# Optimization experiments

Measured on AMD Instinct MI355X. Metric: run time of the kernel, lower is better.

Reference implementation:

```python
import jax, jax.numpy as jnp
import numpy as np

B, D, H = 16384, 1024, 16
HD = D // H
EPS = 1e-5


def setup_inputs() -> dict:
    key = jax.random.key(0)
    ks = jax.random.split(key, 16)
    w = lambda k, shape: jax.random.normal(k, shape, jnp.float32) * 0.02
    return {
        "img_emb": jax.random.normal(ks[0], (B, D), jnp.float32),
        "txt_emb": jax.random.normal(ks[1], (B, D), jnp.float32),
        "route_choice": jax.random.randint(ks[2], (B,), 0, 3, jnp.int32),
        # gate: Linear(2D -> D) + sigmoid
        "Wg": w(ks[3], (2 * D, D)), "bg": jnp.zeros((D,), jnp.float32),
        # MultiheadAttention in/out projections
        "Wqkv": w(ks[4], (D, 3 * D)), "bqkv": jnp.zeros((3 * D,), jnp.float32),
        "Wo": w(ks[5], (D, D)), "bo": jnp.zeros((D,), jnp.float32),
        # LayerNorm
        "gamma": jnp.ones((D,), jnp.float32), "beta": jnp.zeros((D,), jnp.float32),
        # FFN: Linear(D->4D), GELU, Linear(4D->D)
        "Wf1": w(ks[6], (D, 4 * D)), "bf1": jnp.zeros((4 * D,), jnp.float32),
        "Wf2": w(ks[7], (4 * D, D)), "bf2": jnp.zeros((D,), jnp.float32),
    }


def _layernorm(x, gamma, beta):
    mu = jnp.mean(x, axis=-1, keepdims=True)
    var = jnp.mean(jnp.square(x - mu), axis=-1, keepdims=True)
    return (x - mu) * jax.lax.rsqrt(var + EPS) * gamma + beta


def reference(img_emb, txt_emb, route_choice, Wg, bg, Wqkv, bqkv, Wo, bo,
              gamma, beta, Wf1, bf1, Wf2, bf2):
    # Eval mode: energy_loss = 0, no dropout. Routing choice supplied as int input.
    # Compute the 'full' fusion branch densely, then select per sample.
    ri = jnp.concatenate([img_emb, txt_emb], axis=-1)          # [B, 2D]
    gate = jax.nn.sigmoid(ri @ Wg + bg)                        # [B, D]
    fused = gate * img_emb + (1.0 - gate) * txt_emb            # [B, D]

    x = jnp.stack([img_emb, txt_emb], axis=1)                  # [B, 2, D]
    qkv = x @ Wqkv + bqkv                                      # [B, 2, 3D]
    q, k, v = jnp.split(qkv, 3, axis=-1)
    q = q.reshape(B, 2, H, HD)
    k = k.reshape(B, 2, H, HD)
    v = v.reshape(B, 2, H, HD)
    scores = jnp.einsum("bqhd,bkhd->bhqk", q, k) / np.sqrt(HD) # [B, H, 2, 2]
    attn = jax.nn.softmax(scores, axis=-1)
    ctx = jnp.einsum("bhqk,bkhd->bqhd", attn, v).reshape(B, 2, D)
    attn_out = ctx @ Wo + bo                                   # [B, 2, D]

    fused = fused + attn_out.mean(axis=1)
    fused = _layernorm(fused, gamma, beta)
    full_out = jax.nn.gelu(fused @ Wf1 + bf1, approximate=False) @ Wf2 + bf2

    rc = route_choice[:, None]
    out = jnp.where(rc == 0, img_emb, jnp.where(rc == 1, txt_emb, full_out))
    return out
```

## Files before the change

### kernel.cpp

```cpp
#include <hip/hip_runtime.h>
#include <hip/hip_bf16.h>
#include <math.h>

#define NB 16384
#define DIM 1024
#define CAP 6656
#define MT 52
#define MT2 26

using bf16 = __hip_bfloat16;
typedef __attribute__((ext_vector_type(8))) short short8;
typedef __attribute__((ext_vector_type(4))) short short4v;
typedef __attribute__((ext_vector_type(4))) float float4v;

__device__ __forceinline__ void gl_lds16(const void* g, void* l) {
  __builtin_amdgcn_global_load_lds(
      (const __attribute__((address_space(1))) unsigned int*)g,
      (__attribute__((address_space(3))) unsigned int*)l, 16, 0, 0);
}

__device__ __forceinline__ short f2bf(float x) {
  __hip_bfloat16 h = __float2bfloat16(x);
  return *reinterpret_cast<short*>(&h);
}

__device__ __forceinline__ void swz(int bid, int nN, int& m0, int& n0) {
  int x = bid & 7;
  int r = bid >> 3;
  int nl = nN >> 3;
  int nLoc = r % nl;
  int m = r / nl;
  n0 = (x + 8 * nLoc) * 128;
  m0 = m * 128;
}

__device__ __forceinline__ void swz256(int bid, int nN, int& m0, int& n0) {
  int x = bid & 7;
  int r = bid >> 3;
  int nl = nN >> 3;
  n0 = (x + 8 * (r % nl)) * 256;
  m0 = (r / nl) * 256;
}

__device__ __forceinline__ void stage_unit(const bf16* __restrict__ gbase,
                                           int ld, int kc, bf16* ubase, int t) {
#pragma unroll
  for (int j = 0; j < 2; ++j) {
    int ch = t + j * 512;
    int rg = ch >> 6;
    int rl = (ch >> 2) & 15;
    int cs = ((ch & 3) * 8) ^ ((rl & 6) << 2);
    const bf16* src = gbase + (size_t)(rg * 16 + rl) * ld + kc + cs;
    gl_lds16(src, (void*)(ubase + ((t >> 6) << 9) + j * 4096));
  }
}

template <int MODE>
__global__ __launch_bounds__(512, 2) void gemm256(
    const bf16* __restrict__ A0, const bf16* __restrict__ A1,
    const bf16* __restrict__ B0, const bf16* __restrict__ Bg0,
    const bf16* __restrict__ Bg1, const float* __restrict__ bias0,
    const float* __restrict__ bias1, bf16* __restrict__ O0,
    bf16* __restrict__ O1, float* __restrict__ P,
    const int* __restrict__ cntp) {
  const int cnt = *cntp;
  int bid = blockIdx.x;
  int g = 0, sk = 0, m0, n0;
  if constexpr (MODE == 0) {
    g = bid >= 416;
    bid -= g * 416;
    swz256(bid, 16, m0, n0);
  } else if constexpr (MODE == 1) {
    swz256(bid, 16, m0, n0);
  } else {
    sk = bid / 104;
    int rm = bid % 104;
    m0 = (rm >> 2) * 256;
    n0 = (rm & 3) * 256;
  }
  if (m0 >= ((cnt + 255) & ~255)) return;

  constexpr int LDA = (MODE == 2) ? 4096 : 1024;
  constexpr int LDB = (MODE == 2) ? 4096 : 1024;
  constexpr int NK = (MODE == 2) ? 64 : 32;
  const int kb = (MODE == 2) ? sk * 2048 : 0;

  const bf16* Ab;
  const bf16* Bt;
  if constexpr (MODE == 0) {
    Ab = (g ? A1 : A0) + (size_t)m0 * LDA;
    Bt = (n0 < 3072) ? B0 + (size_t)n0 * 1024
                     : (g ? Bg1 : Bg0) + (size_t)(n0 - 3072) * 1024;
  } else {
    Ab = A0 + (size_t)m0 * LDA;
    Bt = B0 + (size_t)n0 * LDB;
  }

  alignas(16) __shared__ bf16 lds[4][2][8192];
  const int t = threadIdx.x;
  const int wave = t >> 6, lane = t & 63;
  const int wm = wave >> 2, wn = wave & 3;
  const int r16 = lane & 15, quad = lane >> 4;
  const int xorv = (quad * 8) ^ ((r16 & 6) << 2);

#pragma unroll
  for (int s = 0; s < 3; ++s) {
    stage_unit(Ab, LDA, kb + s * 32, &lds[s][0][0], t);
    stage_unit(Bt, LDB, kb + s * 32, &lds[s][1][0], t);
  }
  asm volatile("s_waitcnt vmcnt(8)" ::: "memory");
  __builtin_amdgcn_s_barrier();

  float4v acc[8][4] = {};
#pragma unroll 4
  for (int kt = 0; kt < NK; ++kt) {
    const int slot = kt & 3;
    if (kt + 3 < NK) {
      const int sl = (kt + 3) & 3;
      stage_unit(Ab, LDA, kb + (kt + 3) * 32, &lds[sl][0][0], t);
      stage_unit(Bt, LDB, kb + (kt + 3) * 32, &lds[sl][1][0], t);
    }
    const bf16* aU = &lds[slot][0][0];
    const bf16* bU = &lds[slot][1][0];
    short8 av[8], bv[4];
#pragma unroll
    for (int mi = 0; mi < 8; ++mi)
      av[mi] = *(const short8*)(aU + (wm * 128 + mi * 16 + r16) * 32 + xorv);
#pragma unroll
    for (int ni = 0; ni < 4; ++ni)
      bv[ni] = *(const short8*)(bU + (wn * 64 + ni * 16 + r16) * 32 + xorv);
    asm volatile("s_waitcnt lgkmcnt(0)" ::: "memory");
    __builtin_amdgcn_s_setprio(1);
#pragma unroll
    for (int mi = 0; mi < 8; ++mi)
#pragma unroll
      for (int ni = 0; ni < 4; ++ni)
        acc[mi][ni] = __builtin_amdgcn_mfma_f32_16x16x32_bf16(
            av[mi], bv[ni], acc[mi][ni], 0, 0, 0);
    __builtin_amdgcn_s_setprio(0);
    if (kt < NK - 3) {
      asm volatile("s_waitcnt vmcnt(8)" ::: "memory");
    } else if (kt == NK - 3) {
      asm volatile("s_waitcnt vmcnt(4)" ::: "memory");
    } else if (kt == NK - 2) {
      asm volatile("s_waitcnt vmcnt(0)" ::: "memory");
    }
    __builtin_amdgcn_s_barrier();
  }

  const int colb = n0 + wn * 64 + r16;
  if constexpr (MODE == 2) {
    float* out = P + (size_t)sk * CAP * 1024;
#pragma unroll
    for (int nf = 0; nf < 4; ++nf) {
      int gcol = colb + nf * 16;
#pragma unroll
      for (int mf = 0; mf < 8; ++mf)
#pragma unroll
        for (int r = 0; r < 4; ++r) {
          int grow = m0 + wm * 128 + mf * 16 + quad * 4 + r;
          out[(size_t)grow * 1024 + gcol] = acc[mf][nf][r];
        }
    }
  } else {
    const float* bias = (MODE == 0) ? (g ? bias1 : bias0) : bias0;
    bf16* O = (MODE == 0) ? (g ? O1 : O0) : O0;
    float bvv[4];
#pragma unroll
    for (int nf = 0; nf < 4; ++nf) bvv[nf] = bias[colb + nf * 16];
#pragma unroll
    for (int nf = 0; nf < 4; ++nf) {
      int gcol = colb + nf * 16;
#pragma unroll
      for (int mf = 0; mf < 8; ++mf)
#pragma unroll
        for (int r = 0; r < 4; ++r) {
          int grow = m0 + wm * 128 + mf * 16 + quad * 4 + r;
          float v = acc[mf][nf][r] + bvv[nf];
          if constexpr (MODE == 1)
            v = 0.5f * v * (1.f + erff(v * 0.70710678118654752f));
          O[(size_t)grow * 4096 + gcol] = __float2bfloat16(v);
        }
    }
  }
}

__global__ __launch_bounds__(256) void transpose_cast(
    const float* __restrict__ in, bf16* __restrict__ out, int K, int N) {
  __shared__ float tile[32][33];
  int n0 = blockIdx.x * 32, k0 = blockIdx.y * 32;
  int tx = threadIdx.x, ty = threadIdx.y;
#pragma unroll
  for (int i = 0; i < 32; i += 8)
    tile[ty + i][tx] = in[(size_t)(k0 + ty + i) * N + n0 + tx];
  __syncthreads();
#pragma unroll
  for (int i = 0; i < 32; i += 8)
    out[(size_t)(n0 + ty + i) * K + k0 + tx] = __float2bfloat16(tile[tx][ty + i]);
}

__global__ __launch_bounds__(256) void fill_bias(const float* __restrict__ bqkv,
                                                 const float* __restrict__ bg,
                                                 float* __restrict__ biasA,
                                                 float* __restrict__ biasB) {
  int i = blockIdx.x * 256 + threadIdx.x;
  float qv = (i < 3072) ? bqkv[i] : 0.f;
  biasA[i] = qv;
  biasB[i] = (i < 3072) ? qv : bg[i - 3072];
}

__global__ void zero_cnt(int* cnt) { if (threadIdx.x == 0) *cnt = 0; }

__global__ __launch_bounds__(256) void index_build(const int* __restrict__ route,
                                                   int* __restrict__ cnt,
                                                   int* __restrict__ idx,
                                                   int* __restrict__ pos) {
  int r = blockIdx.x * 256 + threadIdx.x;
  if (r < NB && route[r] == 2) {
    int p = atomicAdd(cnt, 1);
    idx[p] = r;
    pos[r] = p;
  }
}

__global__ __launch_bounds__(256) void gather_cast(
    const float* __restrict__ img, const float* __restrict__ txt,
    const int* __restrict__ cnt, const int* __restrict__ idx,
    bf16* __restrict__ xg, bf16* __restrict__ tg) {
  int n = blockIdx.x;
  if (n >= *cnt) return;
  int r = idx[n];
  int c = threadIdx.x * 4;
  float4 vi = *(const float4*)(img + (size_t)r * DIM + c);
  float4 vt = *(const float4*)(txt + (size_t)r * DIM + c);
  short4v pi, pt;
  pi[0] = f2bf(vi.x); pi[1] = f2bf(vi.y); pi[2] = f2bf(vi.z); pi[3] = f2bf(vi.w);
  pt[0] = f2bf(vt.x); pt[1] = f2bf(vt.y); pt[2] = f2bf(vt.z); pt[3] = f2bf(vt.w);
  *(short4v*)(xg + (size_t)n * DIM + c) = pi;
  *(short4v*)(tg + (size_t)n * DIM + c) = pt;
}

__global__ __launch_bounds__(256) void attn_kernel(const bf16* __restrict__ qx,
                                                   const bf16* __restrict__ tx,
                                                   bf16* __restrict__ cmean,
                                                   const int* __restrict__ cntp) {
  const int cnt = *cntp;
  int gw = blockIdx.x * 4 + (threadIdx.x >> 6);
  int lane = threadIdx.x & 63;
  int n = gw >> 4, h = gw & 15;
  if (n >= ((cnt + 127) & ~127)) return;
  const bf16* b0 = qx + (size_t)n * 4096 + h * 64 + lane;
  const bf16* b1 = tx + (size_t)n * 4096 + h * 64 + lane;
  float q0 = __bfloat162float(b0[0]);
  float k0 = __bfloat162float(b0[1024]);
  float v0 = __bfloat162float(b0[2048]);
  float q1 = __bfloat162float(b1[0]);
  float k1 = __bfloat162float(b1[1024]);
  float v1 = __bfloat162float(b1[2048]);
  float s00 = q0 * k0, s01 = q0 * k1, s10 = q1 * k0, s11 = q1 * k1;
#pragma unroll
  for (int d = 32; d > 0; d >>= 1) {
    s00 += __shfl_xor(s00, d);
    s01 += __shfl_xor(s01, d);
    s10 += __shfl_xor(s10, d);
    s11 += __shfl_xor(s11, d);
  }
  const float sc = 0.125f;
  s00 *= sc; s01 *= sc; s10 *= sc; s11 *= sc;
  float m0 = fmaxf(s00, s01), m1 = fmaxf(s10, s11);
  float e00 = expf(s00 - m0), e01 = expf(s01 - m0);
  float e10 = expf(s10 - m1), e11 = expf(s11 - m1);
  float i0 = 1.f / (e00 + e01), i1 = 1.f / (e10 + e11);
  float c0 = (e00 * i0) * v0 + (e01 * i0) * v1;
  float c1 = (e10 * i1) * v0 + (e11 * i1) * v1;
  cmean[(size_t)n * DIM + h * 64 + lane] = __float2bfloat16(0.5f * (c0 + c1));
}

__global__ __launch_bounds__(256) void wo_z_kernel(
    const float* __restrict__ img, const float* __restrict__ txt,
    const bf16* __restrict__ qx, const bf16* __restrict__ tx,
    const bf16* __restrict__ WoT, const float* __restrict__ bg,
    const float* __restrict__ bo, const bf16* __restrict__ cmean,
    bf16* __restrict__ z, const int* __restrict__ cntp, const int* __restrict__ idx) {
  const int cnt = *cntp;
  int m0, n0;
  swz(blockIdx.x, 8, m0, n0);
  if (m0 >= ((cnt + 127) & ~127)) return;
  alignas(16) __shared__ bf16 sA[128 * 32];
  alignas(16) __shared__ bf16 sB[128 * 32];
  const int t = threadIdx.x;
  const int wave = t >> 6, lane = t & 63;
  const int wm = (wave >> 1) * 64, wn = (wave & 1) * 64;
  const int r16 = lane & 15, quad = lane >> 4;

  float4v acc[4][4] = {};
  for (int k0 = 0; k0 < 1024; k0 += 32) {
    if (k0) __syncthreads();
#pragma unroll
    for (int j = 0; j < 2; ++j) {
      int c = t + j * 256;
      int row = c >> 2;
      int kk = k0 + (c & 3) * 8;
      gl_lds16(WoT + (size_t)(n0 + row) * 1024 + kk, (void*)(sB + j * 2048 + wave * 512));
      gl_lds16(cmean + (size_t)(m0 + row) * 1024 + kk, (void*)(sA + j * 2048 + wave * 512));
    }
    __syncthreads();
    short8 af[4], bfr[4];
#pragma unroll
    for (int i = 0; i < 4; ++i) {
      af[i] = *(const short8*)(sA + (wm + i * 16 + r16) * 32 + quad * 8);
      bfr[i] = *(const short8*)(sB + (wn + i * 16 + r16) * 32 + quad * 8);
    }
#pragma unroll
    for (int i = 0; i < 4; ++i)
#pragma unroll
      for (int j = 0; j < 4; ++j)
        acc[i][j] =
            __builtin_amdgcn_mfma_f32_16x16x32_bf16(af[i], bfr[j], acc[i][j], 0, 0, 0);
  }
#pragma unroll
  for (int i = 0; i < 4; ++i)
#pragma unroll
    for (int j = 0; j < 4; ++j) {
      int gcol = n0 + wn + j * 16 + r16;
      float bgv = bg[gcol], bov = bo[gcol];
#pragma unroll
      for (int r = 0; r < 4; ++r) {
        int grow = m0 + wm + i * 16 + quad * 4 + r;
        float zv = 0.f;
        if (grow < cnt) {
          int orow = idx[grow];
          float gp = __bfloat162float(qx[(size_t)grow * 4096 + 3072 + gcol]) +
                     __bfloat162float(tx[(size_t)grow * 4096 + 3072 + gcol]) + bgv;
          float g = 1.f / (1.f + expf(-gp));
          size_t ii = (size_t)orow * DIM + gcol;
          float fm = g * img[ii] + (1.f - g) * txt[ii];
          zv = fm + acc[i][j][r] + bov;
        }
        z[(size_t)grow * DIM + gcol] = __float2bfloat16(zv);
      }
    }
}

__global__ __launch_bounds__(256) void ln_kernel(bf16* __restrict__ z,
                                                 const float* __restrict__ g,
                                                 const float* __restrict__ be,
                                                 const int* __restrict__ cntp) {
  const int cnt = *cntp;
  int b = blockIdx.x, t = threadIdx.x;
  if (b >= ((cnt + 127) & ~127)) return;
  bf16* zr = z + (size_t)b * DIM;
  float v[4];
  float s = 0.f, s2 = 0.f;
#pragma unroll
  for (int i = 0; i < 4; ++i) {
    float x = __bfloat162float(zr[t + 256 * i]);
    v[i] = x; s += x; s2 += x * x;
  }
#pragma unroll
  for (int d = 32; d > 0; d >>= 1) {
    s += __shfl_xor(s, d);
    s2 += __shfl_xor(s2, d);
  }
  __shared__ float rs[4], rs2[4];
  int w = t >> 6, lane = t & 63;
  if (!lane) { rs[w] = s; rs2[w] = s2; }
  __syncthreads();
  s = rs[0] + rs[1] + rs[2] + rs[3];
  s2 = rs2[0] + rs2[1] + rs2[2] + rs2[3];
  float mu = s * (1.f / 1024.f);
  float var = s2 * (1.f / 1024.f) - mu * mu;
  float r = rsqrtf(var + 1e-5f);
#pragma unroll
  for (int i = 0; i < 4; ++i) {
    int c = t + 256 * i;
    zr[c] = __float2bfloat16((v[i] - mu) * r * g[c] + be[c]);
  }
}

__global__ __launch_bounds__(256) void route_out(
    const float* __restrict__ img, const float* __restrict__ txt,
    const int* __restrict__ route, const int* __restrict__ pos,
    const float* __restrict__ parts, const float* __restrict__ bf2,
    float* __restrict__ out) {
  int row = blockIdx.x;
  int rc = route[row];
  int c = threadIdx.x * 4;
  float4 v;
  if (rc == 2) {
    int n = pos[row];
    float4 p0 = *(const float4*)(parts + (size_t)n * 1024 + c);
    float4 p1 = *(const float4*)(parts + (size_t)CAP * 1024 + (size_t)n * 1024 + c);
    float4 b = *(const float4*)(bf2 + c);
    v.x = p0.x + p1.x + b.x;
    v.y = p0.y + p1.y + b.y;
    v.z = p0.z + p1.z + b.z;
    v.w = p0.w + p1.w + b.w;
  } else {
    const float* src = (rc == 0) ? img : txt;
    v = *(const float4*)(src + (size_t)row * DIM + c);
  }
  *(float4*)(out + (size_t)row * DIM + c) = v;
}

extern "C" void kernel_launch(void* const* d_in, const int* in_sizes, int n_in,
                              void* d_out, int out_size, void* d_ws, size_t ws_size,
                              hipStream_t stream) {
  const float* img = (const float*)d_in[0];
  const float* txt = (const float*)d_in[1];
  const int* route = (const int*)d_in[2];
  const float* Wg = (const float*)d_in[3];
  const float* bg = (const float*)d_in[4];
  const float* Wqkv = (const float*)d_in[5];
  const float* bqkv = (const float*)d_in[6];
  const float* Wo = (const float*)d_in[7];
  const float* bo = (const float*)d_in[8];
  const float* gamma = (const float*)d_in[9];
  const float* beta = (const float*)d_in[10];
  const float* Wf1 = (const float*)d_in[11];
  const float* bf1 = (const float*)d_in[12];
  const float* Wf2 = (const float*)d_in[13];
  const float* bf2 = (const float*)d_in[14];

  char* ws = (char*)d_ws;
  size_t off = 0;
  auto alloc = [&](size_t bytes) {
    char* p = ws + off;
    off += (bytes + 255) & ~(size_t)255;
    return p;
  };
  int* cntp = (int*)alloc(256);
  int* idx = (int*)alloc((size_t)NB * 4);
  int* pos = (int*)alloc((size_t)NB * 4);
  float* biasA = (float*)alloc(4096 * 4);
  float* biasB = (float*)alloc(4096 * 4);
  bf16* WqkvT = (bf16*)alloc((size_t)3072 * 1024 * 2);
  bf16* WgTopT = (bf16*)alloc((size_t)1024 * 1024 * 2);
  bf16* WgBotT = (bf16*)alloc((size_t)1024 * 1024 * 2);
  bf16* WoT = (bf16*)alloc((size_t)1024 * 1024 * 2);
  bf16* Wf1T = (bf16*)alloc((size_t)4096 * 1024 * 2);
  bf16* Wf2T = (bf16*)alloc((size_t)1024 * 4096 * 2);
  bf16* xg = (bf16*)alloc((size_t)CAP * 1024 * 2);
  bf16* tg = (bf16*)alloc((size_t)CAP * 1024 * 2);
  bf16* qx = (bf16*)alloc((size_t)CAP * 4096 * 2);
  bf16* tx = (bf16*)alloc((size_t)CAP * 4096 * 2);
  bf16* cmean = (bf16*)alloc((size_t)CAP * 1024 * 2);
  bf16* zb = (bf16*)alloc((size_t)CAP * 1024 * 2);
  bf16* hb = qx;
  float* parts = (float*)tx;

  dim3 tblk(32, 8);
  transpose_cast<<<dim3(3072 / 32, 1024 / 32), tblk, 0, stream>>>(Wqkv, WqkvT, 1024, 3072);
  transpose_cast<<<dim3(1024 / 32, 1024 / 32), tblk, 0, stream>>>(Wg, WgTopT, 1024, 1024);
  transpose_cast<<<dim3(1024 / 32, 1024 / 32), tblk, 0, stream>>>(Wg + 1024 * 1024, WgBotT, 1024, 1024);
  transpose_cast<<<dim3(1024 / 32, 1024 / 32), tblk, 0, stream>>>(Wo, WoT, 1024, 1024);
  transpose_cast<<<dim3(4096 / 32, 1024 / 32), tblk, 0, stream>>>(Wf1, Wf1T, 1024, 4096);
  transpose_cast<<<dim3(1024 / 32, 4096 / 32), tblk, 0, stream>>>(Wf2, Wf2T, 4096, 1024);
  fill_bias<<<16, 256, 0, stream>>>(bqkv, bg, biasA, biasB);

  zero_cnt<<<1, 64, 0, stream>>>(cntp);
  index_build<<<NB / 256, 256, 0, stream>>>(route, cntp, idx, pos);
  gather_cast<<<CAP, 256, 0, stream>>>(img, txt, cntp, idx, xg, tg);

  gemm256<0><<<2 * MT2 * 16, 512, 0, stream>>>(xg, tg, WqkvT, WgTopT, WgBotT,
                                               biasA, biasB, qx, tx, nullptr, cntp);
  attn_kernel<<<CAP * 4, 256, 0, stream>>>(qx, tx, cmean, cntp);
  wo_z_kernel<<<8 * MT, 256, 0, stream>>>(img, txt, qx, tx, WoT, bg, bo, cmean, zb,
                                          cntp, idx);
  ln_kernel<<<CAP, 256, 0, stream>>>(zb, gamma, beta, cntp);
  gemm256<1><<<MT2 * 16, 512, 0, stream>>>(zb, nullptr, Wf1T, nullptr, nullptr,
                                           bf1, nullptr, hb, nullptr, nullptr, cntp);
  gemm256<2><<<MT2 * 4 * 2, 512, 0, stream>>>(hb, nullptr, Wf2T, nullptr, nullptr,
                                              nullptr, nullptr, nullptr, nullptr,
                                              parts, cntp);
  route_out<<<NB, 256, 0, stream>>>(img, txt, route, pos, parts, bf2, (float*)d_out);
}
```

Baseline: 639.1 us.

## Switch GEMM main loop to BK=64 double-buffered tiles with wider swizzle

```diff
diff --git a/kernel.cpp b/kernel.cpp
--- a/kernel.cpp
+++ b/kernel.cpp
@@ -42,17 +42,15 @@
   m0 = (r / nl) * 256;
 }
 
-__device__ __forceinline__ void stage_unit(const bf16* __restrict__ gbase,
-                                           int ld, int kc, bf16* ubase, int t) {
-#pragma unroll
-  for (int j = 0; j < 2; ++j) {
-    int ch = t + j * 512;
-    int rg = ch >> 6;
-    int rl = (ch >> 2) & 15;
-    int cs = ((ch & 3) * 8) ^ ((rl & 6) << 2);
-    const bf16* src = gbase + (size_t)(rg * 16 + rl) * ld + kc + cs;
-    gl_lds16(src, (void*)(ubase + ((t >> 6) << 9) + j * 4096));
-  }
+__device__ __forceinline__ void stage64(const bf16* __restrict__ gbase,
+                                        int ld, int kc, bf16* ubase, int t) {
+  const int rl = t >> 3;
+  const int cs = ((t & 7) ^ (rl & 7)) * 8;
+  const bf16* src0 = gbase + (size_t)rl * ld + kc + cs;
+  bf16* dst0 = ubase + ((t >> 6) << 9);
+#pragma unroll
+  for (int j = 0; j < 4; ++j)
+    gl_lds16(src0 + (size_t)(j * 64) * ld, (void*)(dst0 + j * 4096));
 }
 
 template <int MODE>
@@ -82,7 +80,7 @@
 
   constexpr int LDA = (MODE == 2) ? 4096 : 1024;
   constexpr int LDB = (MODE == 2) ? 4096 : 1024;
-  constexpr int NK = (MODE == 2) ? 64 : 32;
+  constexpr int NK = (MODE == 2) ? 32 : 16;
   const int kb = (MODE == 2) ? sk * 2048 : 0;
 
   const bf16* Ab;
@@ -96,39 +94,37 @@
     Bt = B0 + (size_t)n0 * LDB;
   }
 
-  alignas(16) __shared__ bf16 lds[4][2][8192];
+  alignas(16) __shared__ bf16 lds[2][2][16384];
   const int t = threadIdx.x;
   const int wave = t >> 6, lane = t & 63;
   const int wm = wave >> 2, wn = wave & 3;
   const int r16 = lane & 15, quad = lane >> 4;
-  const int xorv = (quad * 8) ^ ((r16 & 6) << 2);
-
-#pragma unroll
-  for (int s = 0; s < 3; ++s) {
-    stage_unit(Ab, LDA, kb + s * 32, &lds[s][0][0], t);
-    stage_unit(Bt, LDB, kb + s * 32, &lds[s][1][0], t);
-  }
-  asm volatile("s_waitcnt vmcnt(8)" ::: "memory");
+  const int r7 = r16 & 7;
+  const int ck0 = (quad ^ r7) * 8;
+  const int ck1 = ((4 + quad) ^ r7) * 8;
+
+  stage64(Ab, LDA, kb, &lds[0][0][0], t);
+  stage64(Bt, LDB, kb, &lds[0][1][0], t);
+  asm volatile("s_waitcnt vmcnt(0)" ::: "memory");
   __builtin_amdgcn_s_barrier();
 
   float4v acc[8][4] = {};
-#pragma unroll 4
+#pragma unroll 2
   for (int kt = 0; kt < NK; ++kt) {
-    const int slot = kt & 3;
-    if (kt + 3 < NK) {
-      const int sl = (kt + 3) & 3;
-      stage_unit(Ab, LDA, kb + (kt + 3) * 32, &lds[sl][0][0], t);
-      stage_unit(Bt, LDB, kb + (kt + 3) * 32, &lds[sl][1][0], t);
-    }
-    const bf16* aU = &lds[slot][0][0];
-    const bf16* bU = &lds[slot][1][0];
+    const int sl = kt & 1;
+    if (kt + 1 < NK) {
+      stage64(Ab, LDA, kb + (kt + 1) * 64, &lds[sl ^ 1][0][0], t);
+      stage64(Bt, LDB, kb + (kt + 1) * 64, &lds[sl ^ 1][1][0], t);
+    }
+    const bf16* aU = &lds[sl][0][0];
+    const bf16* bU = &lds[sl][1][0];
     short8 av[8], bv[4];
 #pragma unroll
     for (int mi = 0; mi < 8; ++mi)
-      av[mi] = *(const short8*)(aU + (wm * 128 + mi * 16 + r16) * 32 + xorv);
+      av[mi] = *(const short8*)(aU + (wm * 128 + mi * 16 + r16) * 64 + ck0);
 #pragma unroll
     for (int ni = 0; ni < 4; ++ni)
-      bv[ni] = *(const short8*)(bU + (wn * 64 + ni * 16 + r16) * 32 + xorv);
+      bv[ni] = *(const short8*)(bU + (wn * 64 + ni * 16 + r16) * 64 + ck0);
     asm volatile("s_waitcnt lgkmcnt(0)" ::: "memory");
     __builtin_amdgcn_s_setprio(1);
 #pragma unroll
@@ -138,13 +134,22 @@
         acc[mi][ni] = __builtin_amdgcn_mfma_f32_16x16x32_bf16(
             av[mi], bv[ni], acc[mi][ni], 0, 0, 0);
     __builtin_amdgcn_s_setprio(0);
-    if (kt < NK - 3) {
-      asm volatile("s_waitcnt vmcnt(8)" ::: "memory");
-    } else if (kt == NK - 3) {
-      asm volatile("s_waitcnt vmcnt(4)" ::: "memory");
-    } else if (kt == NK - 2) {
-      asm volatile("s_waitcnt vmcnt(0)" ::: "memory");
-    }
+#pragma unroll
+    for (int mi = 0; mi < 8; ++mi)
+      av[mi] = *(const short8*)(aU + (wm * 128 + mi * 16 + r16) * 64 + ck1);
+#pragma unroll
+    for (int ni = 0; ni < 4; ++ni)
+      bv[ni] = *(const short8*)(bU + (wn * 64 + ni * 16 + r16) * 64 + ck1);
+    asm volatile("s_waitcnt lgkmcnt(0)" ::: "memory");
+    __builtin_amdgcn_s_setprio(1);
+#pragma unroll
+    for (int mi = 0; mi < 8; ++mi)
+#pragma unroll
+      for (int ni = 0; ni < 4; ++ni)
+        acc[mi][ni] = __builtin_amdgcn_mfma_f32_16x16x32_bf16(
+            av[mi], bv[ni], acc[mi][ni], 0, 0, 0);
+    __builtin_amdgcn_s_setprio(0);
+    if (kt + 1 < NK) asm volatile("s_waitcnt vmcnt(0)" ::: "memory");
     __builtin_amdgcn_s_barrier();
   }
 
```

New measurement: 616.7 us. 1.04x faster.
